# Kernel optimization log

Hardware: AMD Instinct MI355X
Metric: run time of the kernel (lower is better)

## Reference

```python
import jax, jax.numpy as jnp
import numpy as np
import math

B, S, D = 2, 2048, 2048
H, KVH, HD = 16, 8, 128  # n_heads, n_kv_heads, head_dim
N_REP = H // KVH
ROPE_THETA = 500000.0
NEG_INF = -1e9


def _rope(t, f):
    # t: (B,S,nh,HD) viewed as pairs; f: (S,HD//2,2) = (cos,sin)
    tp = t.reshape(*t.shape[:-1], HD // 2, 2)          # (B,S,nh,HD//2,2)
    fb = f[:, None]                                     # (S,1,HD//2,2)
    row1 = (tp * fb).sum(-1)                            # x0*c + x1*s
    f_rot = jnp.stack([fb[..., 1], -fb[..., 0]], axis=-1)  # (s, -c)
    row0 = (tp * f_rot).sum(-1)                         # x0*s - x1*c
    return jnp.stack([row0, row1], axis=-1).reshape(t.shape)


def setup_inputs() -> dict:
    key = jax.random.key(0)
    ks = jax.random.split(key, 5)
    x = jax.random.normal(ks[0], (B, S, D), dtype=jnp.float32)
    # RoPE table: (S, HD//2, 2) stacked (cos, sin)
    inv_freq = 1.0 / (ROPE_THETA ** (np.arange(0, HD, 2, dtype=np.float32) / HD))
    t = np.arange(S, dtype=np.float32)
    ang = np.outer(t, inv_freq)                         # (S, HD//2)
    freqs_cis = jnp.asarray(np.stack([np.cos(ang), np.sin(ang)], axis=-1))
    # causal additive mask (S,S)
    mask = jnp.where(jnp.triu(jnp.ones((S, S), dtype=bool), k=1), NEG_INF, 0.0).astype(jnp.float32)
    sc = 1.0 / math.sqrt(D)
    wq = jax.random.normal(ks[1], (D, H * HD), dtype=jnp.float32) * sc
    wk = jax.random.normal(ks[2], (D, KVH * HD), dtype=jnp.float32) * sc
    wv = jax.random.normal(ks[3], (D, KVH * HD), dtype=jnp.float32) * sc
    wo = jax.random.normal(ks[4], (H * HD, D), dtype=jnp.float32) * sc
    return {"x": x, "freqs_cis": freqs_cis, "mask": mask, "wq": wq, "wk": wk, "wv": wv, "wo": wo}


def reference(x, freqs_cis, mask, wq, wk, wv, wo):
    bsz, seqlen, _ = x.shape
    xq = (x @ wq).reshape(bsz, seqlen, H, HD)
    xk = (x @ wk).reshape(bsz, seqlen, KVH, HD)
    xv = (x @ wv).reshape(bsz, seqlen, KVH, HD)
    xq = _rope(xq, freqs_cis)
    xk = _rope(xk, freqs_cis)
    keys = jnp.repeat(xk, N_REP, axis=2)                # (B,S,H,HD)
    values = jnp.repeat(xv, N_REP, axis=2)
    q = xq.transpose(0, 2, 1, 3)                        # (B,H,S,HD)
    k = keys.transpose(0, 2, 1, 3)
    v = values.transpose(0, 2, 1, 3)
    scores = jnp.einsum('bhqd,bhkd->bhqk', q, k) / math.sqrt(HD)
    scores = scores + mask                              # broadcast (S,S)
    probs = jax.nn.softmax(scores.astype(jnp.float32), axis=-1).astype(q.dtype)
    out = jnp.einsum('bhqk,bhkd->bhqd', probs, v)
    out = out.transpose(0, 2, 1, 3).reshape(bsz, seqlen, H * HD)
    return out @ wo
```

## Files before the change

### kernel.cpp

```cpp
#include <hip/hip_runtime.h>

typedef short short8 __attribute__((ext_vector_type(8)));
typedef float v4f __attribute__((ext_vector_type(4)));

#define LOG2E 1.4426950408889634f

__device__ __forceinline__ unsigned short f2bf(float f) {
  unsigned int u = __float_as_uint(f);
  u += 0x7fff + ((u >> 16) & 1);
  return (unsigned short)(u >> 16);
}
__device__ __forceinline__ float b2f(unsigned short h) {
  return __uint_as_float(((unsigned int)h) << 16);
}
__device__ __forceinline__ void gl_lds16(const void* g, void* l) {
  __builtin_amdgcn_global_load_lds((const __attribute__((address_space(1))) void*)g,
                                   (__attribute__((address_space(3))) void*)l, 16, 0, 0);
}

__global__ __launch_bounds__(256) void cvt_f32_bf16(const float* __restrict__ src,
                                                    unsigned short* __restrict__ dst, int n) {
  int i = (blockIdx.x * 256 + threadIdx.x) * 4;
  if (i < n) {
    float4 v = *(const float4*)(src + i);
    ushort4 o;
    o.x = f2bf(v.x); o.y = f2bf(v.y); o.z = f2bf(v.z); o.w = f2bf(v.w);
    *(ushort4*)(dst + i) = o;
  }
}

__global__ __launch_bounds__(256) void transpose_f32_bf16(const float* __restrict__ src,
                                                          unsigned short* __restrict__ dst,
                                                          int srcCols) {
  __shared__ float tile[64][65];
  const int c0 = blockIdx.x * 64;
  const int r0 = blockIdx.y * 64;
  const int t = threadIdx.x;
#pragma unroll
  for (int i = 0; i < 16; ++i) {
    int idx = t + i * 256; int r = idx >> 6, c = idx & 63;
    tile[r][c] = src[(size_t)(r0 + r) * srcCols + c0 + c];
  }
  __syncthreads();
#pragma unroll
  for (int i = 0; i < 16; ++i) {
    int idx = t + i * 256; int r = idx >> 6, c = idx & 63;
    dst[(size_t)(c0 + r) * 2048 + r0 + c] = f2bf(tile[c][r]);
  }
}

template <bool OUT_BF16>
__global__ __launch_bounds__(256) void gemm_bt(const unsigned short* __restrict__ A,
                                               const unsigned short* __restrict__ Bt,
                                               void* __restrict__ Cv,
                                               int M, int N, int K) {
  __shared__ __align__(16) unsigned short As[2][128 * 32];
  __shared__ __align__(16) unsigned short Bs[2][128 * 32];
  const int t = threadIdx.x;
  const int wave = t >> 6, lane = t & 63, quad = lane >> 4, l16 = lane & 15;
  const int tm = blockIdx.y * 128, tn = blockIdx.x * 128;
  const int wm = (wave >> 1) * 64, wn = (wave & 1) * 64;
  v4f acc[4][4];
#pragma unroll
  for (int i = 0; i < 4; ++i)
#pragma unroll
    for (int j = 0; j < 4; ++j) acc[i][j] = (v4f){0.f, 0.f, 0.f, 0.f};

  const int swz = (l16 >> 1) & 3;

  const int s0 = t, s1 = 256 + t;
  const unsigned short* pa0 = A + (size_t)(tm + (s0 >> 2)) * K + ((s0 & 3) ^ ((s0 >> 3) & 3)) * 8;
  const unsigned short* pa1 = A + (size_t)(tm + (s1 >> 2)) * K + ((s1 & 3) ^ ((s1 >> 3) & 3)) * 8;
  const unsigned short* pb0 = Bt + (size_t)(tn + (s0 >> 2)) * K + ((s0 & 3) ^ ((s0 >> 3) & 3)) * 8;
  const unsigned short* pb1 = Bt + (size_t)(tn + (s1 >> 2)) * K + ((s1 & 3) ^ ((s1 >> 3) & 3)) * 8;
  const int dOff0 = (wave * 64) * 8;
  const int dOff1 = (256 + wave * 64) * 8;

  gl_lds16(pa0, &As[0][dOff0]); gl_lds16(pa1, &As[0][dOff1]);
  gl_lds16(pb0, &Bs[0][dOff0]); gl_lds16(pb1, &Bs[0][dOff1]);
  pa0 += 32; pa1 += 32; pb0 += 32; pb1 += 32;

  const int nit = K >> 5;
  for (int it = 0; it < nit; ++it) {
    __syncthreads();
    const int cur = it & 1;
    if (it + 1 < nit) {
      const int nxt = cur ^ 1;
      gl_lds16(pa0, &As[nxt][dOff0]); gl_lds16(pa1, &As[nxt][dOff1]);
      gl_lds16(pb0, &Bs[nxt][dOff0]); gl_lds16(pb1, &Bs[nxt][dOff1]);
      pa0 += 32; pa1 += 32; pb0 += 32; pb1 += 32;
    }
    short8 af[4], bf[4];
#pragma unroll
    for (int mt = 0; mt < 4; ++mt)
      af[mt] = *(const short8*)(&As[cur][(wm + mt * 16 + l16) * 32 + (quad ^ swz) * 8]);
#pragma unroll
    for (int nt = 0; nt < 4; ++nt)
      bf[nt] = *(const short8*)(&Bs[cur][(wn + nt * 16 + l16) * 32 + (quad ^ swz) * 8]);
#pragma unroll
    for (int mt = 0; mt < 4; ++mt)
#pragma unroll
      for (int nt = 0; nt < 4; ++nt)
        acc[mt][nt] = __builtin_amdgcn_mfma_f32_16x16x32_bf16(af[mt], bf[nt], acc[mt][nt], 0, 0, 0);
  }

#pragma unroll
  for (int mt = 0; mt < 4; ++mt)
#pragma unroll
    for (int nt = 0; nt < 4; ++nt)
#pragma unroll
      for (int r = 0; r < 4; ++r) {
        int row = tm + wm + mt * 16 + quad * 4 + r;
        int col = tn + wn + nt * 16 + l16;
        float v = acc[mt][nt][r];
        if (OUT_BF16) ((unsigned short*)Cv)[(size_t)row * N + col] = f2bf(v);
        else          ((float*)Cv)[(size_t)row * N + col] = v;
      }
}

template <bool OUT_BF16>
__global__ __launch_bounds__(512, 2) void gemm256(const unsigned short* __restrict__ A,
                                                  const unsigned short* __restrict__ Bt,
                                                  void* __restrict__ Cv,
                                                  int M, int N, int K) {
  __shared__ __align__(16) unsigned short As[2][256 * 64];
  __shared__ __align__(16) unsigned short Bs[2][256 * 64];
  const int t = threadIdx.x;
  const int wave = t >> 6, lane = t & 63, quad = lane >> 4, l16 = lane & 15;
  const int wr = wave >> 2, wc = wave & 3;

  const int gx = N >> 8;
  int id = blockIdx.y * gridDim.x + blockIdx.x;
  const int nwg = gridDim.x * gridDim.y;
  id = (id & 7) * (nwg >> 3) + (id >> 3);
  const int tm = (id / gx) << 8, tn = (id % gx) << 8;

  v4f acc[8][4];
#pragma unroll
  for (int i = 0; i < 8; ++i)
#pragma unroll
    for (int j = 0; j < 4; ++j) acc[i][j] = (v4f){0.f, 0.f, 0.f, 0.f};

  const int s0 = t, s1 = 512 + t;
  const size_t hA = (size_t)128 * K;
  const unsigned short* a0 = A + (size_t)(tm + (s0 >> 3)) * K + ((s0 & 7) ^ ((s0 >> 3) & 7)) * 8;
  const unsigned short* a1 = A + (size_t)(tm + (s1 >> 3)) * K + ((s1 & 7) ^ ((s1 >> 3) & 7)) * 8;
  const unsigned short* b0 = Bt + (size_t)(tn + (s0 >> 3)) * K + ((s0 & 7) ^ ((s0 >> 3) & 7)) * 8;
  const unsigned short* b1 = Bt + (size_t)(tn + (s1 >> 3)) * K + ((s1 & 7) ^ ((s1 >> 3) & 7)) * 8;
  const int d0 = (wave * 64) * 8;
  const int d1 = (512 + wave * 64) * 8;

#define STG_A(buf, h, koff)                                         \
  do {                                                              \
    gl_lds16(a0 + (size_t)(h) * hA + (koff), &As[buf][(h) * 8192 + d0]); \
    gl_lds16(a1 + (size_t)(h) * hA + (koff), &As[buf][(h) * 8192 + d1]); \
  } while (0)
#define STG_B(buf, h, koff)                                         \
  do {                                                              \
    gl_lds16(b0 + (size_t)(h) * hA + (koff), &Bs[buf][(h) * 8192 + d0]); \
    gl_lds16(b1 + (size_t)(h) * hA + (koff), &Bs[buf][(h) * 8192 + d1]); \
  } while (0)

  const int aBase = (wr * 128 + l16) * 64;
  const int bBase = (wc * 64 + l16) * 64;
  const int c0 = (quad ^ (l16 & 7)) * 8;
  const int c1 = ((4 + quad) ^ (l16 & 7)) * 8;

  const int nkt = K >> 6;

  STG_A(0, 0, 0); STG_A(0, 1, 0);
  STG_B(0, 0, 0); STG_B(0, 1, 0);
  STG_B(1, 0, 64); STG_A(1, 0, 64);
  asm volatile("s_waitcnt vmcnt(4)" ::: "memory");
  __builtin_amdgcn_s_barrier();

  short8 af[4][2], bf[4][2];
  for (int kt = 0; kt < nkt; ++kt) {
    const int cur = kt & 1, nxt = cur ^ 1;
    const int koff = kt << 6;

#pragma unroll
    for (int m = 0; m < 4; ++m) {
      af[m][0] = *(const short8*)(&As[cur][aBase + m * 1024 + c0]);
      af[m][1] = *(const short8*)(&As[cur][aBase + m * 1024 + c1]);
    }
#pragma unroll
    for (int n = 0; n < 2; ++n) {
      bf[n][0] = *(const short8*)(&Bs[cur][bBase + n * 1024 + c0]);
      bf[n][1] = *(const short8*)(&Bs[cur][bBase + n * 1024 + c1]);
    }
    if (kt + 1 < nkt) { STG_A(nxt, 1, koff + 64); STG_B(nxt, 1, koff + 64); }
    __builtin_amdgcn_s_barrier();
    asm volatile("s_waitcnt lgkmcnt(0)" ::: "memory");
    __builtin_amdgcn_s_setprio(1);
#pragma unroll
    for (int m = 0; m < 4; ++m)
#pragma unroll
      for (int n = 0; n < 2; ++n) {
        acc[m][n] = __builtin_amdgcn_mfma_f32_16x16x32_bf16(af[m][0], bf[n][0], acc[m][n], 0, 0, 0);
        acc[m][n] = __builtin_amdgcn_mfma_f32_16x16x32_bf16(af[m][1], bf[n][1], acc[m][n], 0, 0, 0);
      }
    __builtin_amdgcn_s_setprio(0);
    __builtin_amdgcn_s_barrier();

#pragma unroll
    for (int n = 2; n < 4; ++n) {
      bf[n][0] = *(const short8*)(&Bs[cur][bBase + n * 1024 + c0]);
      bf[n][1] = *(const short8*)(&Bs[cur][bBase + n * 1024 + c1]);
    }
    __builtin_amdgcn_s_barrier();
    asm volatile("s_waitcnt lgkmcnt(0)" ::: "memory");
    __builtin_amdgcn_s_setprio(1);
#pragma unroll
    for (int m = 0; m < 4; ++m)
#pragma unroll
      for (int n = 2; n < 4; ++n) {
        acc[m][n] = __builtin_amdgcn_mfma_f32_16x16x32_bf16(af[m][0], bf[n][0], acc[m][n], 0, 0, 0);
        acc[m][n] = __builtin_amdgcn_mfma_f32_16x16x32_bf16(af[m][1], bf[n][1], acc[m][n], 0, 0, 0);
      }
    __builtin_amdgcn_s_setprio(0);
    __builtin_amdgcn_s_barrier();

#pragma unroll
    for (int m = 0; m < 4; ++m) {
      af[m][0] = *(const short8*)(&As[cur][aBase + (4 + m) * 1024 + c0]);
      af[m][1] = *(const short8*)(&As[cur][aBase + (4 + m) * 1024 + c1]);
    }
    if (kt + 2 < nkt) STG_B(cur, 0, koff + 128);
    __builtin_amdgcn_s_barrier();
    asm volatile("s_waitcnt lgkmcnt(0)" ::: "memory");
    __builtin_amdgcn_s_setprio(1);
#pragma unroll
    for (int m = 0; m < 4; ++m)
#pragma unroll
      for (int n = 0; n < 2; ++n) {
        acc[4 + m][n] = __builtin_amdgcn_mfma_f32_16x16x32_bf16(af[m][0], bf[n][0], acc[4 + m][n], 0, 0, 0);
        acc[4 + m][n] = __builtin_amdgcn_mfma_f32_16x16x32_bf16(af[m][1], bf[n][1], acc[4 + m][n], 0, 0, 0);
      }
    __builtin_amdgcn_s_setprio(0);
    __builtin_amdgcn_s_barrier();

    if (kt + 2 < nkt) {
      STG_A(cur, 0, koff + 128);
      asm volatile("s_waitcnt vmcnt(4)" ::: "memory");
    } else {
      asm volatile("s_waitcnt vmcnt(0)" ::: "memory");
    }
    __builtin_amdgcn_s_barrier();
    __builtin_amdgcn_s_setprio(1);
#pragma unroll
    for (int m = 0; m < 4; ++m)
#pragma unroll
      for (int n = 2; n < 4; ++n) {
        acc[4 + m][n] = __builtin_amdgcn_mfma_f32_16x16x32_bf16(af[m][0], bf[n][0], acc[4 + m][n], 0, 0, 0);
        acc[4 + m][n] = __builtin_amdgcn_mfma_f32_16x16x32_bf16(af[m][1], bf[n][1], acc[4 + m][n], 0, 0, 0);
      }
    __builtin_amdgcn_s_setprio(0);
    __builtin_amdgcn_s_barrier();
  }
#undef STG_A
#undef STG_B

#pragma unroll
  for (int mf = 0; mf < 8; ++mf)
#pragma unroll
    for (int nf = 0; nf < 4; ++nf)
#pragma unroll
      for (int r = 0; r < 4; ++r) {
        int row = tm + wr * 128 + mf * 16 + quad * 4 + r;
        int col = tn + wc * 64 + nf * 16 + l16;
        float v = acc[mf][nf][r];
        if (OUT_BF16) ((unsigned short*)Cv)[(size_t)row * N + col] = f2bf(v);
        else          ((float*)Cv)[(size_t)row * N + col] = v;
      }
}

__global__ __launch_bounds__(256) void rope_k(unsigned short* __restrict__ qkv,
                                              const float* __restrict__ freqs) {
  const int bs = blockIdx.x;
  const int s = bs & 2047;
  const float qscale = 0.08838834764831845f;
  unsigned int* row = (unsigned int*)(qkv + (size_t)bs * 4096);
  const float2* fr2 = (const float2*)(freqs + s * 128);
#pragma unroll
  for (int k = 0; k < 6; ++k) {
    int d = threadIdx.x + k * 256;
    float sc = (d < 1024) ? qscale : 1.0f;
    float2 cs = fr2[d & 63];
    unsigned int w = row[d];
    float x0 = b2f((unsigned short)(w & 0xffffu));
    float x1 = b2f((unsigned short)(w >> 16));
    float y0 = (x0 * cs.y - x1 * cs.x) * sc;
    float y1 = (x0 * cs.x + x1 * cs.y) * sc;
    row[d] = ((unsigned int)f2bf(y1) << 16) | (unsigned int)f2bf(y0);
  }
}

__global__ __launch_bounds__(256) void transpose_v(const unsigned short* __restrict__ qkv,
                                                   unsigned short* __restrict__ vt) {
  __shared__ unsigned short tile[64][65];
  const int s0 = blockIdx.x * 64, d0 = blockIdx.y * 64;
  const int bk = blockIdx.z; const int b = bk >> 3, kv = bk & 7;
  const int t = threadIdx.x;
#pragma unroll
  for (int i = 0; i < 16; ++i) {
    int idx = t + i * 256; int r = idx >> 6, c = idx & 63;
    tile[r][c] = qkv[(size_t)(b * 2048 + s0 + r) * 4096 + 3072 + kv * 128 + d0 + c];
  }
  __syncthreads();
#pragma unroll
  for (int i = 0; i < 16; ++i) {
    int idx = t + i * 256; int r = idx >> 6, c = idx & 63;
    vt[((size_t)bk * 128 + d0 + r) * 2048 + s0 + c] = tile[c][r];
  }
}

__global__ __launch_bounds__(256) void attn_k(const unsigned short* __restrict__ qkv,
                                              const unsigned short* __restrict__ vt,
                                              unsigned short* __restrict__ Ob) {
  __shared__ __align__(16) unsigned short Ks[2][64 * 128];
  __shared__ __align__(16) unsigned short Vs[2][128 * 64];
  __shared__ __align__(16) unsigned short Ps[4][16 * 64];
  const int t = threadIdx.x, wave = t >> 6, lane = t & 63, quad = lane >> 4, l16 = lane & 15;
  const int jpair = blockIdx.x, h = blockIdx.y, b = blockIdx.z;
  const int kv = h >> 1;

  auto stage = [&](int jt, int buf) {
#pragma unroll
    for (int issue = 0; issue < 4; ++issue) {
      int s = issue * 256 + t;
      gl_lds16(qkv + (size_t)(b * 2048 + jt * 64 + (s >> 4)) * 4096 + 2048 + kv * 128 +
                   (((s & 15) ^ ((s >> 4) & 15)) * 8),
               &Ks[buf][(issue * 256 + wave * 64) * 8]);
      gl_lds16(vt + ((size_t)(b * 8 + kv) * 128 + (s >> 3)) * 2048 + jt * 64 +
                   (((s & 7) ^ ((s >> 3) & 7)) * 8),
               &Vs[buf][(issue * 256 + wave * 64) * 8]);
    }
  };

  for (int pass = 0; pass < 2; ++pass) {
    const int qblk = (pass == 0) ? jpair : 31 - jpair;
    const int q0 = qblk * 64;

    stage(0, 0);

    short8 qf[4];
    {
      const unsigned short* qp =
          qkv + (size_t)(b * 2048 + q0 + wave * 16 + l16) * 4096 + h * 128 + quad * 8;
#pragma unroll
      for (int kc = 0; kc < 4; ++kc) qf[kc] = *(const short8*)(qp + kc * 32);
    }
    v4f oa[8];
#pragma unroll
    for (int i = 0; i < 8; ++i) oa[i] = (v4f){0.f, 0.f, 0.f, 0.f};
    float m_s = -3.0e38f, l_s = 0.f;

    for (int jt = 0; jt <= qblk; ++jt) {
      const int cur = jt & 1;
      if (jt < qblk) {
        stage(jt + 1, cur ^ 1);
        asm volatile("s_waitcnt vmcnt(8)" ::: "memory");
      } else {
        asm volatile("s_waitcnt vmcnt(0)" ::: "memory");
      }
      __builtin_amdgcn_s_barrier();

      v4f st[4];
#pragma unroll
      for (int mt = 0; mt < 4; ++mt) st[mt] = (v4f){0.f, 0.f, 0.f, 0.f};
#pragma unroll
      for (int kc = 0; kc < 4; ++kc)
#pragma unroll
        for (int mt = 0; mt < 4; ++mt) {
          short8 kf =
              *(const short8*)(&Ks[cur][(mt * 16 + l16) * 128 + (((kc * 4 + quad) ^ l16) * 8)]);
          st[mt] = __builtin_amdgcn_mfma_f32_16x16x32_bf16(kf, qf[kc], st[mt], 0, 0, 0);
        }

      float mx = -3.0e38f;
      if (jt == qblk) {
#pragma unroll
        for (int mt = 0; mt < 4; ++mt)
#pragma unroll
          for (int r = 0; r < 4; ++r) {
            float v = st[mt][r];
            if (mt * 16 + quad * 4 + r > wave * 16 + l16) v = -1.0e30f;
            st[mt][r] = v;
            mx = fmaxf(mx, v);
          }
      } else {
#pragma unroll
        for (int mt = 0; mt < 4; ++mt)
#pragma unroll
          for (int r = 0; r < 4; ++r) mx = fmaxf(mx, st[mt][r]);
      }
      mx = fmaxf(mx, __shfl_xor(mx, 16));
      mx = fmaxf(mx, __shfl_xor(mx, 32));

      if (__ballot(mx > m_s + 8.0f)) {
        float mn = fmaxf(m_s, mx);
        float alpha = exp2f((m_s - mn) * LOG2E);
        m_s = mn;
        float a_q[4];
#pragma unroll
        for (int r = 0; r < 4; ++r) a_q[r] = __shfl(alpha, quad * 4 + r);
#pragma unroll
        for (int nt = 0; nt < 8; ++nt)
#pragma unroll
          for (int r = 0; r < 4; ++r) oa[nt][r] *= a_q[r];
        l_s *= alpha;
      }
      float lt = 0.f;
#pragma unroll
      for (int mt = 0; mt < 4; ++mt)
#pragma unroll
        for (int r = 0; r < 4; ++r) {
          float p = exp2f((st[mt][r] - m_s) * LOG2E);
          st[mt][r] = p;
          lt += p;
        }
      lt += __shfl_xor(lt, 16);
      lt += __shfl_xor(lt, 32);
      l_s += lt;

#pragma unroll
      for (int mt = 0; mt < 4; ++mt) {
        int pcp = ((mt * 2 + (quad >> 1)) ^ (l16 & 7));
        ushort4 w;
        w.x = f2bf(st[mt][0]); w.y = f2bf(st[mt][1]);
        w.z = f2bf(st[mt][2]); w.w = f2bf(st[mt][3]);
        *(ushort4*)(&Ps[wave][l16 * 64 + pcp * 8 + (quad & 1) * 4]) = w;
      }
      asm volatile("s_waitcnt lgkmcnt(0)" ::: "memory");

      short8 pf[2];
#pragma unroll
      for (int kc2 = 0; kc2 < 2; ++kc2)
        pf[kc2] = *(const short8*)(&Ps[wave][l16 * 64 + (((kc2 * 4 + quad) ^ (l16 & 7)) * 8)]);
#pragma unroll
      for (int nt = 0; nt < 8; ++nt)
#pragma unroll
        for (int kc2 = 0; kc2 < 2; ++kc2) {
          short8 vf = *(const short8*)(&Vs[cur][(nt * 16 + l16) * 64 +
                                                (((kc2 * 4 + quad) ^ (l16 & 7)) * 8)]);
          oa[nt] = __builtin_amdgcn_mfma_f32_16x16x32_bf16(pf[kc2], vf, oa[nt], 0, 0, 0);
        }
      __builtin_amdgcn_s_barrier();
    }

    float inv[4];
#pragma unroll
    for (int r = 0; r < 4; ++r) inv[r] = 1.0f / __shfl(l_s, quad * 4 + r);
#pragma unroll
    for (int r = 0; r < 4; ++r) {
      int row = b * 2048 + q0 + wave * 16 + quad * 4 + r;
#pragma unroll
      for (int nt = 0; nt < 8; ++nt)
        Ob[(size_t)row * 2048 + h * 128 + nt * 16 + l16] = f2bf(oa[nt][r] * inv[r]);
    }
    __syncthreads();
  }
}

extern "C" void kernel_launch(void* const* d_in, const int* in_sizes, int n_in,
                              void* d_out, int out_size, void* d_ws, size_t ws_size,
                              hipStream_t stream) {
  (void)in_sizes; (void)n_in; (void)out_size; (void)ws_size;
  const float* x  = (const float*)d_in[0];
  const float* fr = (const float*)d_in[1];
  const float* wq = (const float*)d_in[3];
  const float* wk = (const float*)d_in[4];
  const float* wv = (const float*)d_in[5];
  const float* wo = (const float*)d_in[6];
  float* out = (float*)d_out;

  char* ws = (char*)d_ws;
  unsigned short* Xb    = (unsigned short*)(ws);
  unsigned short* WqkvT = (unsigned short*)(ws + (size_t)(16u << 20));
  unsigned short* WoT   = (unsigned short*)(ws + (size_t)(32u << 20));
  unsigned short* QKV   = (unsigned short*)(ws + (size_t)(40u << 20));
  unsigned short* Vt    = (unsigned short*)(ws);
  unsigned short* Ob    = (unsigned short*)(ws + (size_t)(16u << 20));

  cvt_f32_bf16<<<8192, 256, 0, stream>>>(x, Xb, 2 * 2048 * 2048);
  transpose_f32_bf16<<<dim3(32, 32), 256, 0, stream>>>(wq, WqkvT, 2048);
  transpose_f32_bf16<<<dim3(16, 32), 256, 0, stream>>>(wk, WqkvT + (size_t)2048 * 2048, 1024);
  transpose_f32_bf16<<<dim3(16, 32), 256, 0, stream>>>(wv, WqkvT + (size_t)3072 * 2048, 1024);
  transpose_f32_bf16<<<dim3(32, 32), 256, 0, stream>>>(wo, WoT, 2048);
  gemm256<true><<<dim3(16, 16), 512, 0, stream>>>(Xb, WqkvT, QKV, 4096, 4096, 2048);
  rope_k<<<4096, 256, 0, stream>>>(QKV, fr);
  transpose_v<<<dim3(32, 2, 16), 256, 0, stream>>>(QKV, Vt);
  attn_k<<<dim3(16, 16, 2), 256, 0, stream>>>(QKV, Vt, Ob);
  gemm_bt<false><<<dim3(16, 32), 256, 0, stream>>>(Ob, WoT, out, 4096, 2048, 2048);
}
```

Measured before the change: 351.6 us.

## Rewrite attention with 128x128 tiles and 32x32x16 MFMA, P kept in registers

Result: slower. 363.5 us (+3.4%).

```diff
diff --git a/kernel.cpp b/kernel.cpp
--- a/kernel.cpp
+++ b/kernel.cpp
@@ -2,6 +2,7 @@
 
 typedef short short8 __attribute__((ext_vector_type(8)));
 typedef float v4f __attribute__((ext_vector_type(4)));
+typedef float v16f __attribute__((ext_vector_type(16)));
 
 #define LOG2E 1.4426950408889634f
 
@@ -315,150 +316,161 @@
   }
 }
 
-__global__ __launch_bounds__(256) void attn_k(const unsigned short* __restrict__ qkv,
-                                              const unsigned short* __restrict__ vt,
-                                              unsigned short* __restrict__ Ob) {
-  __shared__ __align__(16) unsigned short Ks[2][64 * 128];
-  __shared__ __align__(16) unsigned short Vs[2][128 * 64];
-  __shared__ __align__(16) unsigned short Ps[4][16 * 64];
-  const int t = threadIdx.x, wave = t >> 6, lane = t & 63, quad = lane >> 4, l16 = lane & 15;
-  const int jpair = blockIdx.x, h = blockIdx.y, b = blockIdx.z;
-  const int kv = h >> 1;
+__global__ __launch_bounds__(256, 1) void attn_k(const unsigned short* __restrict__ qkv,
+                                                 const unsigned short* __restrict__ vt,
+                                                 unsigned short* __restrict__ Ob) {
+  __shared__ __align__(16) unsigned short Ks[2][128 * 128];
+  __shared__ __align__(16) unsigned short Vs[2][128 * 128];
+  const int t = threadIdx.x, wave = t >> 6, lane = t & 63;
+  const int l31 = lane & 31, hh2 = lane >> 5;
+  const int jp = blockIdx.x, hd = blockIdx.y, b = blockIdx.z;
+  const int kv = hd >> 1;
 
   auto stage = [&](int jt, int buf) {
 #pragma unroll
-    for (int issue = 0; issue < 4; ++issue) {
+    for (int issue = 0; issue < 8; ++issue) {
       int s = issue * 256 + t;
-      gl_lds16(qkv + (size_t)(b * 2048 + jt * 64 + (s >> 4)) * 4096 + 2048 + kv * 128 +
-                   (((s & 15) ^ ((s >> 4) & 15)) * 8),
+      int row = s >> 4;
+      int src = ((s & 15) ^ (row & 15)) * 8;
+      gl_lds16(qkv + (size_t)(b * 2048 + jt * 128 + row) * 4096 + 2048 + kv * 128 + src,
                &Ks[buf][(issue * 256 + wave * 64) * 8]);
-      gl_lds16(vt + ((size_t)(b * 8 + kv) * 128 + (s >> 3)) * 2048 + jt * 64 +
-                   (((s & 7) ^ ((s >> 3) & 7)) * 8),
+      gl_lds16(vt + ((size_t)(b * 8 + kv) * 128 + row) * 2048 + jt * 128 + src,
                &Vs[buf][(issue * 256 + wave * 64) * 8]);
     }
   };
 
   for (int pass = 0; pass < 2; ++pass) {
-    const int qblk = (pass == 0) ? jpair : 31 - jpair;
-    const int q0 = qblk * 64;
-
+    const int qblk = (pass == 0) ? jp : 15 - jp;
+    const int q0 = qblk * 128;
+    const int qrel = wave * 32 + l31;
+    const int qrow = q0 + qrel;
+
+    short8 qf[8];
+    {
+      const unsigned short* qp = qkv + (size_t)(b * 2048 + qrow) * 4096 + hd * 128 + hh2 * 8;
+#pragma unroll
+      for (int ks = 0; ks < 8; ++ks) qf[ks] = *(const short8*)(qp + ks * 16);
+    }
     stage(0, 0);
 
-    short8 qf[4];
-    {
-      const unsigned short* qp =
-          qkv + (size_t)(b * 2048 + q0 + wave * 16 + l16) * 4096 + h * 128 + quad * 8;
-#pragma unroll
-      for (int kc = 0; kc < 4; ++kc) qf[kc] = *(const short8*)(qp + kc * 32);
-    }
-    v4f oa[8];
-#pragma unroll
-    for (int i = 0; i < 8; ++i) oa[i] = (v4f){0.f, 0.f, 0.f, 0.f};
+    v16f oa[4];
+#pragma unroll
+    for (int i = 0; i < 4; ++i)
+#pragma unroll
+      for (int r = 0; r < 16; ++r) oa[i][r] = 0.f;
     float m_s = -3.0e38f, l_s = 0.f;
 
-    for (int jt = 0; jt <= qblk; ++jt) {
+    const int ntl = qblk + 1;
+    for (int jt = 0; jt < ntl; ++jt) {
       const int cur = jt & 1;
-      if (jt < qblk) {
+      if (jt + 1 < ntl) {
         stage(jt + 1, cur ^ 1);
-        asm volatile("s_waitcnt vmcnt(8)" ::: "memory");
+        asm volatile("s_waitcnt vmcnt(16)" ::: "memory");
       } else {
         asm volatile("s_waitcnt vmcnt(0)" ::: "memory");
       }
       __builtin_amdgcn_s_barrier();
 
-      v4f st[4];
-#pragma unroll
-      for (int mt = 0; mt < 4; ++mt) st[mt] = (v4f){0.f, 0.f, 0.f, 0.f};
-#pragma unroll
-      for (int kc = 0; kc < 4; ++kc)
-#pragma unroll
-        for (int mt = 0; mt < 4; ++mt) {
-          short8 kf =
-              *(const short8*)(&Ks[cur][(mt * 16 + l16) * 128 + (((kc * 4 + quad) ^ l16) * 8)]);
-          st[mt] = __builtin_amdgcn_mfma_f32_16x16x32_bf16(kf, qf[kc], st[mt], 0, 0, 0);
+      v16f st[4];
+#pragma unroll
+      for (int i = 0; i < 4; ++i)
+#pragma unroll
+        for (int r = 0; r < 16; ++r) st[i][r] = 0.f;
+#pragma unroll
+      for (int ks = 0; ks < 8; ++ks)
+#pragma unroll
+        for (int kt = 0; kt < 4; ++kt) {
+          int row = kt * 32 + l31;
+          short8 kf = *(const short8*)(
+              &Ks[cur][row * 128 + (((ks * 2 + hh2) ^ (row & 15)) * 8)]);
+          st[kt] = __builtin_amdgcn_mfma_f32_32x32x16_bf16(kf, qf[ks], st[kt], 0, 0, 0);
         }
 
       float mx = -3.0e38f;
       if (jt == qblk) {
 #pragma unroll
-        for (int mt = 0; mt < 4; ++mt)
-#pragma unroll
-          for (int r = 0; r < 4; ++r) {
-            float v = st[mt][r];
-            if (mt * 16 + quad * 4 + r > wave * 16 + l16) v = -1.0e30f;
-            st[mt][r] = v;
+        for (int kt = 0; kt < 4; ++kt)
+#pragma unroll
+          for (int r = 0; r < 16; ++r) {
+            int key = kt * 32 + (r & 3) + 8 * (r >> 2) + 4 * hh2;
+            float v = st[kt][r];
+            if (key > qrel) v = -1.0e30f;
+            st[kt][r] = v;
             mx = fmaxf(mx, v);
           }
       } else {
 #pragma unroll
-        for (int mt = 0; mt < 4; ++mt)
-#pragma unroll
-          for (int r = 0; r < 4; ++r) mx = fmaxf(mx, st[mt][r]);
-      }
-      mx = fmaxf(mx, __shfl_xor(mx, 16));
+        for (int kt = 0; kt < 4; ++kt)
+#pragma unroll
+          for (int r = 0; r < 16; ++r) mx = fmaxf(mx, st[kt][r]);
+      }
       mx = fmaxf(mx, __shfl_xor(mx, 32));
 
       if (__ballot(mx > m_s + 8.0f)) {
         float mn = fmaxf(m_s, mx);
         float alpha = exp2f((m_s - mn) * LOG2E);
         m_s = mn;
-        float a_q[4];
-#pragma unroll
-        for (int r = 0; r < 4; ++r) a_q[r] = __shfl(alpha, quad * 4 + r);
-#pragma unroll
-        for (int nt = 0; nt < 8; ++nt)
-#pragma unroll
-          for (int r = 0; r < 4; ++r) oa[nt][r] *= a_q[r];
+#pragma unroll
+        for (int i = 0; i < 4; ++i)
+#pragma unroll
+          for (int r = 0; r < 16; ++r) oa[i][r] *= alpha;
         l_s *= alpha;
       }
+
       float lt = 0.f;
-#pragma unroll
-      for (int mt = 0; mt < 4; ++mt)
-#pragma unroll
-        for (int r = 0; r < 4; ++r) {
-          float p = exp2f((st[mt][r] - m_s) * LOG2E);
-          st[mt][r] = p;
-          lt += p;
+      unsigned int PD[4][8];
+#pragma unroll
+      for (int kt = 0; kt < 4; ++kt)
+#pragma unroll
+        for (int j = 0; j < 8; ++j) {
+          float p0 = exp2f((st[kt][2 * j]     - m_s) * LOG2E);
+          float p1 = exp2f((st[kt][2 * j + 1] - m_s) * LOG2E);
+          lt += p0 + p1;
+          unsigned int pd;
+          asm("v_cvt_pk_bf16_f32 %0, %1, %2" : "=v"(pd) : "v"(p0), "v"(p1));
+          PD[kt][j] = pd;
         }
-      lt += __shfl_xor(lt, 16);
       lt += __shfl_xor(lt, 32);
       l_s += lt;
 
-#pragma unroll
-      for (int mt = 0; mt < 4; ++mt) {
-        int pcp = ((mt * 2 + (quad >> 1)) ^ (l16 & 7));
-        ushort4 w;
-        w.x = f2bf(st[mt][0]); w.y = f2bf(st[mt][1]);
-        w.z = f2bf(st[mt][2]); w.w = f2bf(st[mt][3]);
-        *(ushort4*)(&Ps[wave][l16 * 64 + pcp * 8 + (quad & 1) * 4]) = w;
-      }
-      asm volatile("s_waitcnt lgkmcnt(0)" ::: "memory");
-
-      short8 pf[2];
-#pragma unroll
-      for (int kc2 = 0; kc2 < 2; ++kc2)
-        pf[kc2] = *(const short8*)(&Ps[wave][l16 * 64 + (((kc2 * 4 + quad) ^ (l16 & 7)) * 8)]);
-#pragma unroll
-      for (int nt = 0; nt < 8; ++nt)
-#pragma unroll
-        for (int kc2 = 0; kc2 < 2; ++kc2) {
-          short8 vf = *(const short8*)(&Vs[cur][(nt * 16 + l16) * 64 +
-                                                (((kc2 * 4 + quad) ^ (l16 & 7)) * 8)]);
-          oa[nt] = __builtin_amdgcn_mfma_f32_16x16x32_bf16(pf[kc2], vf, oa[nt], 0, 0, 0);
+      unsigned int XD[4][8];
+#pragma unroll
+      for (int kt = 0; kt < 4; ++kt)
+#pragma unroll
+        for (int j = 0; j < 8; ++j) XD[kt][j] = __shfl_xor(PD[kt][j], 32);
+
+#pragma unroll
+      for (int ks = 0; ks < 8; ++ks) {
+        const int tt = ks >> 1, w4 = (ks & 1) * 4;
+        union { unsigned int u[4]; short8 s8; } pf;
+        pf.u[0] = hh2 ? XD[tt][w4 + 2] : PD[tt][w4 + 0];
+        pf.u[1] = hh2 ? XD[tt][w4 + 3] : PD[tt][w4 + 1];
+        pf.u[2] = hh2 ? PD[tt][w4 + 2] : XD[tt][w4 + 0];
+        pf.u[3] = hh2 ? PD[tt][w4 + 3] : XD[tt][w4 + 1];
+#pragma unroll
+        for (int dt = 0; dt < 4; ++dt) {
+          int row = dt * 32 + l31;
+          short8 vf = *(const short8*)(
+              &Vs[cur][row * 128 + (((ks * 2 + hh2) ^ (row & 15)) * 8)]);
+          oa[dt] = __builtin_amdgcn_mfma_f32_32x32x16_bf16(vf, pf.s8, oa[dt], 0, 0, 0);
         }
+      }
       __builtin_amdgcn_s_barrier();
     }
 
-    float inv[4];
-#pragma unroll
-    for (int r = 0; r < 4; ++r) inv[r] = 1.0f / __shfl(l_s, quad * 4 + r);
-#pragma unroll
-    for (int r = 0; r < 4; ++r) {
-      int row = b * 2048 + q0 + wave * 16 + quad * 4 + r;
-#pragma unroll
-      for (int nt = 0; nt < 8; ++nt)
-        Ob[(size_t)row * 2048 + h * 128 + nt * 16 + l16] = f2bf(oa[nt][r] * inv[r]);
-    }
+    float inv = 1.0f / l_s;
+    unsigned short* orow = Ob + (size_t)(b * 2048 + qrow) * 2048 + hd * 128;
+#pragma unroll
+    for (int dt = 0; dt < 4; ++dt)
+#pragma unroll
+      for (int g = 0; g < 4; ++g) {
+        ushort4 wv;
+        wv.x = f2bf(oa[dt][4 * g + 0] * inv);
+        wv.y = f2bf(oa[dt][4 * g + 1] * inv);
+        wv.z = f2bf(oa[dt][4 * g + 2] * inv);
+        wv.w = f2bf(oa[dt][4 * g + 3] * inv);
+        *(ushort4*)(orow + dt * 32 + 8 * g + 4 * hh2) = wv;
+      }
     __syncthreads();
   }
 }
@@ -491,6 +503,6 @@
   gemm256<true><<<dim3(16, 16), 512, 0, stream>>>(Xb, WqkvT, QKV, 4096, 4096, 2048);
   rope_k<<<4096, 256, 0, stream>>>(QKV, fr);
   transpose_v<<<dim3(32, 2, 16), 256, 0, stream>>>(QKV, Vt);
-  attn_k<<<dim3(16, 16, 2), 256, 0, stream>>>(QKV, Vt, Ob);
+  attn_k<<<dim3(8, 16, 2), 256, 0, stream>>>(QKV, Vt, Ob);
   gemm_bt<false><<<dim3(16, 32), 256, 0, stream>>>(Ob, WoT, out, 4096, 2048, 2048);
 }
```
